# Kernel optimization log

Measured on AMD Instinct MI355X. Metric: run time of the kernel, lower is better.

Reference implementation:

```python
import jax, jax.numpy as jnp
import numpy as np

C = 256
CQ = C // 4


def setup_inputs() -> dict:
    key = jax.random.key(0)
    ks = jax.random.split(key, 7)
    B, H, W = 4, 64, 64
    x = jax.random.normal(ks[0], (B, C, H, W), dtype=jnp.float32)
    s = 1.0 / np.sqrt(C)
    Wq = jax.random.normal(ks[1], (CQ, C), dtype=jnp.float32) * s
    bq = jnp.zeros((CQ,), dtype=jnp.float32)
    Wk = jax.random.normal(ks[2], (CQ, C), dtype=jnp.float32) * s
    bk = jnp.zeros((CQ,), dtype=jnp.float32)
    Wv = jax.random.normal(ks[3], (C, C), dtype=jnp.float32) * s
    bv = jnp.zeros((C,), dtype=jnp.float32)
    gamma = jnp.zeros((1,), dtype=jnp.float32)
    return {"x": x, "Wq": Wq, "bq": bq, "Wk": Wk, "bk": bk,
            "Wv": Wv, "bv": bv, "gamma": gamma}


def reference(x, Wq, bq, Wk, bk, Wv, bv, gamma):
    B, Cc, Hh, Ww = x.shape
    N = Hh * Ww
    xf = x.reshape(B, Cc, N)                      # [B, C, N]
    # 1x1 convs are channel-mixing matmuls
    q = jnp.einsum('oc,bcn->bon', Wq, xf) + bq[None, :, None]   # [B, C/4, N]
    k = jnp.einsum('oc,bcn->bon', Wk, xf) + bk[None, :, None]   # [B, C/4, N]
    v = jnp.einsum('oc,bcn->bon', Wv, xf) + bv[None, :, None]   # [B, C, N]
    energy = jnp.einsum('bci,bcj->bij', q, k)     # [B, N, N] (unscaled)
    attn = jax.nn.softmax(energy, axis=-1)
    out = jnp.einsum('bcj,bij->bci', v, attn)     # [B, C, N]
    out = out.reshape(B, Cc, Hh, Ww)
    return gamma[0] * out + x
```

## Files before the change

### kernel.cpp

```cpp
#include <hip/hip_runtime.h>
#include <hip/hip_bf16.h>

typedef unsigned short u16;
typedef unsigned int u32;
typedef float f32x4 __attribute__((ext_vector_type(4)));
typedef short s16x8 __attribute__((ext_vector_type(8)));

#define MFMA16(a, b, c) __builtin_amdgcn_mfma_f32_16x16x32_bf16(a, b, c, 0, 0, 0)

#define NN 4096
#define CC 256
#define CQ 64

__device__ __forceinline__ u16 f2bf(float x) {
    union { float f; u32 u; } v; v.f = x;
    return (u16)((v.u + 0x7FFFu + ((v.u >> 16) & 1u)) >> 16);
}
__device__ __forceinline__ float bf2f(u16 u) {
    union { u32 u; float f; } v; v.u = ((u32)u) << 16;
    return v.f;
}
__device__ __forceinline__ void gll16(const void* g, void* l) {
    __builtin_amdgcn_global_load_lds(
        (const __attribute__((address_space(1))) void*)g,
        (__attribute__((address_space(3))) void*)l, 16, 0, 0);
}

__global__ __launch_bounds__(256) void prep(
    const float* __restrict__ x, const float* __restrict__ Wq,
    const float* __restrict__ Wk, const float* __restrict__ Wv,
    u16* __restrict__ xT, u16* __restrict__ wbf)
{
    const int bid = blockIdx.x, t = threadIdx.x;
    if (bid < 1024) {
        __shared__ float tile[64 * 65];
        const int b = bid >> 8, ctile = (bid >> 6) & 3, ntile = bid & 63;
        const int c0 = ctile * 64, n0 = ntile * 64;
        const int cw = t >> 4, nj = (t & 15) * 4;
        for (int it = 0; it < 4; it++) {
            const int ci = it * 16 + cw;
            const float4 v4 = *(const float4*)(x + ((size_t)(b * CC + c0 + ci)) * NN + n0 + nj);
            tile[(nj + 0) * 65 + ci] = v4.x;
            tile[(nj + 1) * 65 + ci] = v4.y;
            tile[(nj + 2) * 65 + ci] = v4.z;
            tile[(nj + 3) * 65 + ci] = v4.w;
        }
        __syncthreads();
        const int r = t >> 2, c16 = (t & 3) * 16;
        union { u16 h[16]; uint4 q[2]; } pk;
        for (int j = 0; j < 16; j++) pk.h[j] = f2bf(tile[r * 65 + c16 + j]);
        u16* dst = xT + ((size_t)(b * NN + n0 + r)) * CC + c0 + c16;
        *(uint4*)dst = pk.q[0];
        *(uint4*)(dst + 8) = pk.q[1];
    } else {
        const int flat = (bid - 1024) * 1024 + t * 4;
        const int o = flat >> 8, c = flat & 255;
        const float* src = (o < 64)  ? (Wq + (size_t)o * CC + c)
                         : (o < 128) ? (Wk + (size_t)(o - 64) * CC + c)
                                     : (Wv + (size_t)(o - 128) * CC + c);
        const float4 v4 = *(const float4*)src;
        union { u16 h[4]; uint2 d; } pk;
        pk.h[0] = f2bf(v4.x); pk.h[1] = f2bf(v4.y);
        pk.h[2] = f2bf(v4.z); pk.h[3] = f2bf(v4.w);
        *(uint2*)(wbf + (size_t)o * CC + c) = pk.d;
    }
}

__global__ __launch_bounds__(512, 4) void qkv(
    const u16* __restrict__ xT, const u16* __restrict__ wbf,
    const float* __restrict__ bq, const float* __restrict__ bk,
    const float* __restrict__ bv,
    u16* __restrict__ qT, u16* __restrict__ kT, u16* __restrict__ v)
{
    __shared__ __align__(16) u16 sm[384 * 64 + 32 * 64];
    u16* Ws = sm;
    u16* Xs = sm + 384 * 64;

    const int bid = blockIdx.x;
    const int b = bid >> 7, n0 = (bid & 127) * 32;
    const int t = threadIdx.x, lane = t & 63, w = t >> 6;
    const int col = lane & 15, quad = lane >> 4;

    f32x4 acc[3][2];
    for (int i = 0; i < 3; i++) { acc[i][0] = f32x4{0,0,0,0}; acc[i][1] = f32x4{0,0,0,0}; }

    for (int cc = 0; cc < 4; cc++) {
        const int c0 = cc * 64;
        for (int m = 0; m < 6; m++) {
            const int g = m * 512 + t;
            const int row = g >> 3, ch = g & 7;
            gll16(wbf + (size_t)row * CC + c0 + ((ch ^ (row & 7)) * 8), Ws + g * 8);
        }
        if (w < 4) {
            const int g = w * 64 + lane;
            const int n = g >> 3, ch = g & 7;
            gll16(xT + ((size_t)(b * NN + n0 + n)) * CC + c0 + ((ch ^ (n & 7)) * 8),
                  Xs + g * 8);
        }
        __syncthreads();
        for (int kk = 0; kk < 2; kk++) {
            s16x8 bx[2];
            for (int nt2 = 0; nt2 < 2; nt2++) {
                const int n = nt2 * 16 + col;
                bx[nt2] = *(const s16x8*)&Xs[n * 64 + (((kk * 4 + quad) ^ (n & 7)) * 8)];
            }
            for (int ot = 0; ot < 3; ot++) {
                const int row = w * 48 + ot * 16 + col;
                const s16x8 a = *(const s16x8*)&Ws[row * 64 + (((kk * 4 + quad) ^ (row & 7)) * 8)];
                acc[ot][0] = MFMA16(a, bx[0], acc[ot][0]);
                acc[ot][1] = MFMA16(a, bx[1], acc[ot][1]);
            }
        }
        __syncthreads();
    }
    for (int ot = 0; ot < 3; ot++) {
        const int og = w * 48 + ot * 16 + quad * 4;
        for (int nt2 = 0; nt2 < 2; nt2++) {
            const int n = n0 + nt2 * 16 + col;
            if (og < 64) {
                union { u16 h[4]; uint2 d; } pk;
                for (int r = 0; r < 4; r++) pk.h[r] = f2bf(acc[ot][nt2][r] + bq[og + r]);
                *(uint2*)(qT + ((size_t)(b * NN + n)) * CQ + og) = pk.d;
            } else if (og < 128) {
                union { u16 h[4]; uint2 d; } pk;
                for (int r = 0; r < 4; r++) pk.h[r] = f2bf(acc[ot][nt2][r] + bk[og - 64 + r]);
                *(uint2*)(kT + ((size_t)(b * NN + n)) * CQ + (og - 64)) = pk.d;
            } else {
                for (int r = 0; r < 4; r++)
                    v[((size_t)(b * CC + og - 128 + r)) * NN + n] =
                        f2bf(acc[ot][nt2][r] + bv[og - 128 + r]);
            }
        }
    }
}

__global__ __launch_bounds__(512, 4) void flash_attn(
    const u16* __restrict__ qT, const u16* __restrict__ kT,
    const u16* __restrict__ v,
    u16* __restrict__ Op0, float* __restrict__ Op1,
    float* __restrict__ lws)
{
    __shared__ __align__(16) u16 sm[25600];
    __shared__ float ls[2][64];

    const int bid = blockIdx.x;
    const int p = bid & 7;
    const int b = p >> 1, jh = p & 1;
    const int n0 = (bid >> 3) * 64;
    const int jb = jh * 2048;
    const int t = threadIdx.x;
    const int lane = t & 63, wv = t >> 6;
    const int col = lane & 15, quad = lane >> 4;
    const int strip = wv & 3, jhi = wv >> 2;
    const int ih = wv >> 2, cq = wv & 3;

    s16x8 aq[2];
    {
        const u16* qp = qT + ((size_t)(b * NN + n0 + strip * 16 + col)) * CQ + quad * 8;
        aq[0] = *(const s16x8*)qp;
        aq[1] = *(const s16x8*)(qp + 32);
    }

    f32x4 o_[2][4];
    for (int i = 0; i < 2; i++) for (int j = 0; j < 4; j++) o_[i][j] = f32x4{0,0,0,0};
    float lac[4] = {0.f, 0.f, 0.f, 0.f};

    const int kg = wv * 64 + lane;
    const int krow = kg >> 3;
    const u16* ksrc = kT + ((size_t)(b * NN + jb + krow)) * CQ + (((kg & 7) ^ (krow & 7)) * 8);
    const int kdo = kg * 8;
    const u16* vsrc[2];
    int vdo[2];
    for (int m = 0; m < 2; m++) {
        const int g = m * 512 + t;
        const int row = g >> 2;
        vdo[m] = g * 8;
        vsrc[m] = v + ((size_t)(b * CC + row)) * NN + jb + (g & 3) * 8;
    }

    auto issueK = [&](int jt, int kb) {
        if (wv < 4) gll16(ksrc + (size_t)jt * 32 * CQ, sm + kb * 2048 + kdo);
    };
    auto issueV = [&](int jt, int vb) {
        u16* base = sm + 4096 + vb * 8192;
        for (int m = 0; m < 2; m++)
            gll16(vsrc[m] + jt * 32, base + vdo[m]);
    };
    auto S_phase = [&](int kb, int pb) {
        const u16* Kb = sm + kb * 2048;
        u16* Pb = sm + 20480 + pb * 2560;
        f32x4 s = f32x4{0,0,0,0};
        for (int kk = 0; kk < 2; kk++) {
            const int jrow = jhi * 16 + col;
            const s16x8 bk_ = *(const s16x8*)
                &Kb[jrow * 64 + (((kk * 4 + quad) ^ (jrow & 7)) * 8)];
            s = MFMA16(aq[kk], bk_, s);
        }
        for (int r = 0; r < 4; r++) {
            const float pv = __expf(fminf(s[r], 60.f));
            lac[r] += pv;
            Pb[(strip * 16 + quad * 4 + r) * 40 + jhi * 16 + col] = f2bf(pv);
        }
    };
    auto PV_phase = [&](int pb, int vb) {
        const u16* Pb = sm + 20480 + pb * 2560;
        const u16* Vb = sm + 4096 + vb * 8192;
        s16x8 pa[2];
        for (int it2 = 0; it2 < 2; it2++)
            pa[it2] = *(const s16x8*)&Pb[((ih * 2 + it2) * 16 + col) * 40 + quad * 8];
        for (int ct = 0; ct < 4; ct++) {
            const int c = cq * 64 + ct * 16 + col;
            const s16x8 bv_ = *(const s16x8*)&Vb[c * 32 + quad * 8];
            o_[0][ct] = MFMA16(pa[0], bv_, o_[0][ct]);
            o_[1][ct] = MFMA16(pa[1], bv_, o_[1][ct]);
        }
    };

    issueK(0, 0);
    issueV(0, 0);
    issueK(1, 1);
    __syncthreads();
    S_phase(0, 0);

    int vcur = 0, pcur = 0;
    for (int m = 0; m < 64; m++) {
        __syncthreads();
        issueV((m + 1 < 64) ? m + 1 : 63, vcur ^ 1);
        issueK((m + 2 < 64) ? m + 2 : 63, m & 1);
        PV_phase(pcur, vcur);
        if (m < 63) S_phase((m + 1) & 1, pcur ^ 1);
        vcur ^= 1; pcur ^= 1;
    }

    for (int r = 0; r < 4; r++) {
        float lv = lac[r];
        lv += __shfl_xor(lv, 1, 64);
        lv += __shfl_xor(lv, 2, 64);
        lv += __shfl_xor(lv, 4, 64);
        lv += __shfl_xor(lv, 8, 64);
        lac[r] = lv;
    }
    if (col == 0)
        for (int r = 0; r < 4; r++)
            ls[jhi][strip * 16 + quad * 4 + r] = lac[r];
    __syncthreads();
    if (t < 64)
        lws[(size_t)jh * 4 * NN + (size_t)b * NN + n0 + t] = ls[0][t] + ls[1][t];

    float* Tf = (float*)sm;
    u16*  Tu = sm;
    for (int rd = 0; rd < 2; rd++) {
        if ((cq >> 1) == rd) {
            const int cl = (cq & 1) * 64;
            for (int it2 = 0; it2 < 2; it2++) {
                const int ib = (ih * 2 + it2) * 16 + quad * 4;
                for (int ct = 0; ct < 4; ct++) {
                    const int c = cl + ct * 16 + col;
                    if (jh == 0) {
                        union { u16 h[4]; uint2 d; } pk;
                        for (int r = 0; r < 4; r++) pk.h[r] = f2bf(o_[it2][ct][r]);
                        *(uint2*)&Tu[c * 136 + ib] = pk.d;
                    } else {
                        *(float2*)&Tf[c * 68 + ib] = float2{o_[it2][ct][0], o_[it2][ct][1]};
                        *(float2*)&Tf[c * 68 + ib + 2] = float2{o_[it2][ct][2], o_[it2][ct][3]};
                    }
                }
            }
        }
        __syncthreads();
        const int cl = t >> 2, i0 = (t & 3) * 16;
        const int c = rd * 128 + cl;
        if (jh == 0) {
            u16* dst = Op0 + ((size_t)(b * CC + c)) * NN + n0 + i0;
            *(uint4*)dst       = *(const uint4*)&Tu[cl * 136 + i0];
            *(uint4*)(dst + 8) = *(const uint4*)&Tu[cl * 136 + i0 + 8];
        } else {
            float* dst = Op1 + ((size_t)(b * CC + c)) * NN + n0 + i0;
            for (int k = 0; k < 4; k++)
                *(float4*)(dst + k * 4) = *(const float4*)&Tf[cl * 68 + i0 + k * 4];
        }
        __syncthreads();
    }
}

__global__ __launch_bounds__(256) void combine(
    const float* __restrict__ x, const u16* __restrict__ Op0,
    const float* __restrict__ lws, const float* __restrict__ gamma,
    float* __restrict__ out)
{
    const size_t idx = ((size_t)blockIdx.x * 256 + threadIdx.x) * 4;
    const int b = (int)(idx >> 20);
    const int n = (int)(idx & (NN - 1));
    const float g = gamma[0];
    const float4 xv = *(const float4*)(x + idx);
    const float4 o1 = *(const float4*)(out + idx);
    const u16* o0p = Op0 + idx;
    const float4 l0 = *(const float4*)(lws + (size_t)b * NN + n);
    const float4 l1 = *(const float4*)(lws + (size_t)4 * NN + (size_t)b * NN + n);
    float4 r;
    r.x = xv.x + g * (bf2f(o0p[0]) + o1.x) / (l0.x + l1.x);
    r.y = xv.y + g * (bf2f(o0p[1]) + o1.y) / (l0.y + l1.y);
    r.z = xv.z + g * (bf2f(o0p[2]) + o1.z) / (l0.z + l1.z);
    r.w = xv.w + g * (bf2f(o0p[3]) + o1.w) / (l0.w + l1.w);
    *(float4*)(out + idx) = r;
}

extern "C" void kernel_launch(void* const* d_in, const int* in_sizes, int n_in,
                              void* d_out, int out_size, void* d_ws, size_t ws_size,
                              hipStream_t stream)
{
    const float* x     = (const float*)d_in[0];
    const float* Wq    = (const float*)d_in[1];
    const float* bq    = (const float*)d_in[2];
    const float* Wk    = (const float*)d_in[3];
    const float* bk    = (const float*)d_in[4];
    const float* Wv    = (const float*)d_in[5];
    const float* bv    = (const float*)d_in[6];
    const float* gamma = (const float*)d_in[7];
    float* out = (float*)d_out;

    u16* xT  = (u16*)d_ws;
    u16* wbf = xT  + (size_t)4 * NN * CC;
    u16* qTw = wbf + (size_t)384 * CC;
    u16* kTw = qTw + (size_t)4 * NN * CQ;
    u16* vw  = kTw + (size_t)4 * NN * CQ;
    u16* Op0 = xT;
    float* lws = (float*)wbf;

    prep<<<1120, 256, 0, stream>>>(x, Wq, Wk, Wv, xT, wbf);
    qkv<<<512, 512, 0, stream>>>(xT, wbf, bq, bk, bv, qTw, kTw, vw);
    flash_attn<<<512, 512, 0, stream>>>(qTw, kTw, vw, Op0, out, lws);
    combine<<<4096, 256, 0, stream>>>(x, Op0, lws, gamma, out);
}
```

Before: 169.9 us.

## Fuse all four kernels into a persistent megakernel with grid barriers

Merges prep, qkv, flash attention and combine into one persistent kernel of 512 blocks, separated by atomic-counter grid barriers, so three launch gaps and kernel tails disappear. It also XOR-swizzles the V tile in LDS to cut bank conflicts, and switches P to truncating bf16 conversion to save ALU work. The barrier relies on all 512 blocks being co-resident; if they are not, the kernel deadlocks. The work is also redistributed differently in the prep and combine phases.

```diff
diff --git a/kernel.cpp b/kernel.cpp
--- a/kernel.cpp
+++ b/kernel.cpp
@@ -11,10 +11,15 @@
 #define NN 4096
 #define CC 256
 #define CQ 64
+#define NBLK 512
 
 __device__ __forceinline__ u16 f2bf(float x) {
     union { float f; u32 u; } v; v.f = x;
     return (u16)((v.u + 0x7FFFu + ((v.u >> 16) & 1u)) >> 16);
+}
+__device__ __forceinline__ u16 f2bf_t(float x) {
+    union { float f; u32 u; } v; v.f = x;
+    return (u16)(v.u >> 16);
 }
 __device__ __forceinline__ float bf2f(u16 u) {
     union { u32 u; float f; } v; v.u = ((u32)u) << 16;
@@ -26,19 +31,28 @@
         (__attribute__((address_space(3))) void*)l, 16, 0, 0);
 }
 
-__global__ __launch_bounds__(256) void prep(
-    const float* __restrict__ x, const float* __restrict__ Wq,
-    const float* __restrict__ Wk, const float* __restrict__ Wv,
-    u16* __restrict__ xT, u16* __restrict__ wbf)
-{
-    const int bid = blockIdx.x, t = threadIdx.x;
-    if (bid < 1024) {
-        __shared__ float tile[64 * 65];
-        const int b = bid >> 8, ctile = (bid >> 6) & 3, ntile = bid & 63;
+__device__ __forceinline__ void gbar(int* cnt) {
+    __syncthreads();
+    if (threadIdx.x == 0) {
+        __hip_atomic_fetch_add(cnt, 1, __ATOMIC_RELEASE, __HIP_MEMORY_SCOPE_AGENT);
+        while (__hip_atomic_load(cnt, __ATOMIC_ACQUIRE, __HIP_MEMORY_SCOPE_AGENT) < NBLK)
+            __builtin_amdgcn_s_sleep(2);
+    }
+    __syncthreads();
+}
+
+__device__ void phase_prep(const float* __restrict__ x, const float* __restrict__ Wq,
+                           const float* __restrict__ Wk, const float* __restrict__ Wv,
+                           u16* __restrict__ xT, u16* __restrict__ wbf, u16* SMEM)
+{
+    const int t = threadIdx.x;
+    float* tile = (float*)SMEM;
+    for (int u = blockIdx.x; u < 1024; u += NBLK) {
+        const int b = u >> 8, ctile = (u >> 6) & 3, ntile = u & 63;
         const int c0 = ctile * 64, n0 = ntile * 64;
-        const int cw = t >> 4, nj = (t & 15) * 4;
-        for (int it = 0; it < 4; it++) {
-            const int ci = it * 16 + cw;
+        for (int it = 0; it < 2; it++) {
+            const int idx = it * 512 + t;
+            const int ci = idx >> 4, nj = (idx & 15) * 4;
             const float4 v4 = *(const float4*)(x + ((size_t)(b * CC + c0 + ci)) * NN + n0 + nj);
             tile[(nj + 0) * 65 + ci] = v4.x;
             tile[(nj + 1) * 65 + ci] = v4.y;
@@ -46,14 +60,14 @@
             tile[(nj + 3) * 65 + ci] = v4.w;
         }
         __syncthreads();
-        const int r = t >> 2, c16 = (t & 3) * 16;
-        union { u16 h[16]; uint4 q[2]; } pk;
-        for (int j = 0; j < 16; j++) pk.h[j] = f2bf(tile[r * 65 + c16 + j]);
-        u16* dst = xT + ((size_t)(b * NN + n0 + r)) * CC + c0 + c16;
-        *(uint4*)dst = pk.q[0];
-        *(uint4*)(dst + 8) = pk.q[1];
-    } else {
-        const int flat = (bid - 1024) * 1024 + t * 4;
+        const int r = t >> 3, c8 = (t & 7) * 8;
+        union { u16 h[8]; uint4 q; } pk;
+        for (int j = 0; j < 8; j++) pk.h[j] = f2bf(tile[r * 65 + c8 + j]);
+        *(uint4*)(xT + ((size_t)(b * NN + n0 + r)) * CC + c0 + c8) = pk.q;
+        __syncthreads();
+    }
+    if (blockIdx.x < 48) {
+        const int flat = blockIdx.x * 2048 + t * 4;
         const int o = flat >> 8, c = flat & 255;
         const float* src = (o < 64)  ? (Wq + (size_t)o * CC + c)
                          : (o < 128) ? (Wk + (size_t)(o - 64) * CC + c)
@@ -66,15 +80,14 @@
     }
 }
 
-__global__ __launch_bounds__(512, 4) void qkv(
-    const u16* __restrict__ xT, const u16* __restrict__ wbf,
-    const float* __restrict__ bq, const float* __restrict__ bk,
-    const float* __restrict__ bv,
-    u16* __restrict__ qT, u16* __restrict__ kT, u16* __restrict__ v)
-{
-    __shared__ __align__(16) u16 sm[384 * 64 + 32 * 64];
-    u16* Ws = sm;
-    u16* Xs = sm + 384 * 64;
+__device__ void phase_qkv(const u16* __restrict__ xT, const u16* __restrict__ wbf,
+                          const float* __restrict__ bq, const float* __restrict__ bk,
+                          const float* __restrict__ bv,
+                          u16* __restrict__ qT, u16* __restrict__ kT,
+                          u16* __restrict__ v, u16* SMEM)
+{
+    u16* Ws = SMEM;
+    u16* Xs = SMEM + 384 * 64;
 
     const int bid = blockIdx.x;
     const int b = bid >> 7, n0 = (bid & 127) * 32;
@@ -134,14 +147,13 @@
     }
 }
 
-__global__ __launch_bounds__(512, 4) void flash_attn(
-    const u16* __restrict__ qT, const u16* __restrict__ kT,
-    const u16* __restrict__ v,
-    u16* __restrict__ Op0, float* __restrict__ Op1,
-    float* __restrict__ lws)
-{
-    __shared__ __align__(16) u16 sm[25600];
-    __shared__ float ls[2][64];
+__device__ void phase_flash(const u16* __restrict__ qT, const u16* __restrict__ kT,
+                            const u16* __restrict__ v,
+                            u16* __restrict__ Op0, float* __restrict__ Op1,
+                            float* __restrict__ lws, u16* SMEM)
+{
+    u16* sm = SMEM;
+    float* ls = (float*)(SMEM + 25600);
 
     const int bid = blockIdx.x;
     const int p = bid & 7;
@@ -153,6 +165,7 @@
     const int col = lane & 15, quad = lane >> 4;
     const int strip = wv & 3, jhi = wv >> 2;
     const int ih = wv >> 2, cq = wv & 3;
+    const int key2 = (col >> 1) & 3;
 
     s16x8 aq[2];
     {
@@ -174,8 +187,9 @@
     for (int m = 0; m < 2; m++) {
         const int g = m * 512 + t;
         const int row = g >> 2;
+        const int chc = (g & 3) ^ ((row >> 1) & 3);
         vdo[m] = g * 8;
-        vsrc[m] = v + ((size_t)(b * CC + row)) * NN + jb + (g & 3) * 8;
+        vsrc[m] = v + ((size_t)(b * CC + row)) * NN + jb + chc * 8;
     }
 
     auto issueK = [&](int jt, int kb) {
@@ -199,7 +213,7 @@
         for (int r = 0; r < 4; r++) {
             const float pv = __expf(fminf(s[r], 60.f));
             lac[r] += pv;
-            Pb[(strip * 16 + quad * 4 + r) * 40 + jhi * 16 + col] = f2bf(pv);
+            Pb[(strip * 16 + quad * 4 + r) * 40 + jhi * 16 + col] = f2bf_t(pv);
         }
     };
     auto PV_phase = [&](int pb, int vb) {
@@ -210,7 +224,7 @@
             pa[it2] = *(const s16x8*)&Pb[((ih * 2 + it2) * 16 + col) * 40 + quad * 8];
         for (int ct = 0; ct < 4; ct++) {
             const int c = cq * 64 + ct * 16 + col;
-            const s16x8 bv_ = *(const s16x8*)&Vb[c * 32 + quad * 8];
+            const s16x8 bv_ = *(const s16x8*)&Vb[c * 32 + ((quad ^ key2) * 8)];
             o_[0][ct] = MFMA16(pa[0], bv_, o_[0][ct]);
             o_[1][ct] = MFMA16(pa[1], bv_, o_[1][ct]);
         }
@@ -242,10 +256,10 @@
     }
     if (col == 0)
         for (int r = 0; r < 4; r++)
-            ls[jhi][strip * 16 + quad * 4 + r] = lac[r];
+            ls[jhi * 64 + strip * 16 + quad * 4 + r] = lac[r];
     __syncthreads();
     if (t < 64)
-        lws[(size_t)jh * 4 * NN + (size_t)b * NN + n0 + t] = ls[0][t] + ls[1][t];
+        lws[(size_t)jh * 4 * NN + (size_t)b * NN + n0 + t] = ls[t] + ls[64 + t];
 
     float* Tf = (float*)sm;
     u16*  Tu = sm;
@@ -283,26 +297,46 @@
     }
 }
 
-__global__ __launch_bounds__(256) void combine(
-    const float* __restrict__ x, const u16* __restrict__ Op0,
-    const float* __restrict__ lws, const float* __restrict__ gamma,
-    float* __restrict__ out)
-{
-    const size_t idx = ((size_t)blockIdx.x * 256 + threadIdx.x) * 4;
-    const int b = (int)(idx >> 20);
-    const int n = (int)(idx & (NN - 1));
+__device__ void phase_combine(const float* __restrict__ x, const u16* __restrict__ Op0,
+                              const float* __restrict__ lws, const float* __restrict__ gamma,
+                              float* __restrict__ out)
+{
     const float g = gamma[0];
-    const float4 xv = *(const float4*)(x + idx);
-    const float4 o1 = *(const float4*)(out + idx);
-    const u16* o0p = Op0 + idx;
-    const float4 l0 = *(const float4*)(lws + (size_t)b * NN + n);
-    const float4 l1 = *(const float4*)(lws + (size_t)4 * NN + (size_t)b * NN + n);
-    float4 r;
-    r.x = xv.x + g * (bf2f(o0p[0]) + o1.x) / (l0.x + l1.x);
-    r.y = xv.y + g * (bf2f(o0p[1]) + o1.y) / (l0.y + l1.y);
-    r.z = xv.z + g * (bf2f(o0p[2]) + o1.z) / (l0.z + l1.z);
-    r.w = xv.w + g * (bf2f(o0p[3]) + o1.w) / (l0.w + l1.w);
-    *(float4*)(out + idx) = r;
+    for (int pass = 0; pass < 4; pass++) {
+        const size_t idx = ((size_t)pass * 262144 + (size_t)blockIdx.x * 512 + threadIdx.x) * 4;
+        const int b = (int)(idx >> 20);
+        const int n = (int)(idx & (NN - 1));
+        const float4 xv = *(const float4*)(x + idx);
+        const float4 o1 = *(const float4*)(out + idx);
+        const uint2 o0 = *(const uint2*)(Op0 + idx);
+        const float4 l0 = *(const float4*)(lws + (size_t)b * NN + n);
+        const float4 l1 = *(const float4*)(lws + (size_t)4 * NN + (size_t)b * NN + n);
+        float4 r;
+        r.x = xv.x + g * (bf2f((u16)(o0.x & 0xffff))  + o1.x) / (l0.x + l1.x);
+        r.y = xv.y + g * (bf2f((u16)(o0.x >> 16))     + o1.y) / (l0.y + l1.y);
+        r.z = xv.z + g * (bf2f((u16)(o0.y & 0xffff))  + o1.z) / (l0.z + l1.z);
+        r.w = xv.w + g * (bf2f((u16)(o0.y >> 16))     + o1.w) / (l0.w + l1.w);
+        *(float4*)(out + idx) = r;
+    }
+}
+
+__global__ __launch_bounds__(512, 4) void pam_mega(
+    const float* __restrict__ x, const float* __restrict__ Wq,
+    const float* __restrict__ bq, const float* __restrict__ Wk,
+    const float* __restrict__ bk, const float* __restrict__ Wv,
+    const float* __restrict__ bv, const float* __restrict__ gamma,
+    u16* xT, u16* wbf, u16* qT, u16* kT, u16* v,
+    float* lws, int* ctr, float* out)
+{
+    __shared__ __align__(16) u16 SMEM[26624];
+
+    phase_prep(x, Wq, Wk, Wv, xT, wbf, SMEM);
+    gbar(ctr + 0);
+    phase_qkv(xT, wbf, bq, bk, bv, qT, kT, v, SMEM);
+    gbar(ctr + 1);
+    phase_flash(qT, kT, v, xT, out, lws, SMEM);
+    gbar(ctr + 2);
+    phase_combine(x, xT, lws, gamma, out);
 }
 
 extern "C" void kernel_launch(void* const* d_in, const int* in_sizes, int n_in,
@@ -321,14 +355,13 @@
 
     u16* xT  = (u16*)d_ws;
     u16* wbf = xT  + (size_t)4 * NN * CC;
-    u16* qTw = wbf + (size_t)384 * CC;
-    u16* kTw = qTw + (size_t)4 * NN * CQ;
-    u16* vw  = kTw + (size_t)4 * NN * CQ;
-    u16* Op0 = xT;
+    u16* qT  = wbf + (size_t)384 * CC;
+    u16* kT  = qT  + (size_t)4 * NN * CQ;
+    u16* vw  = kT  + (size_t)4 * NN * CQ;
+    int* ctr = (int*)(vw + (size_t)4 * CC * NN);
     float* lws = (float*)wbf;
 
-    prep<<<1120, 256, 0, stream>>>(x, Wq, Wk, Wv, xT, wbf);
-    qkv<<<512, 512, 0, stream>>>(xT, wbf, bq, bk, bv, qTw, kTw, vw);
-    flash_attn<<<512, 512, 0, stream>>>(qTw, kTw, vw, Op0, out, lws);
-    combine<<<4096, 256, 0, stream>>>(x, Op0, lws, gamma, out);
-}
+    hipMemsetAsync(ctr, 0, 3 * sizeof(int), stream);
+    pam_mega<<<NBLK, 512, 0, stream>>>(x, Wq, bq, Wk, bk, Wv, bv, gamma,
+                                       xT, wbf, qT, kT, vw, lws, ctr, out);
+}
```

Result: slower. 371.6 us (+118.7%).

## Fuse combine into flash_attn via inter-block flag handoff, swizzle V LDS

Applied to the files above, without the earlier changes.

Removes the separate combine kernel. The jh=1 block waits on a per-tile flag released by the jh=0 block, then merges both partial outputs, normalises by the summed row sums, applies gamma and adds x, writing the final output directly. This drops the fp32 partial round-trip through global memory and one kernel launch. It also XOR-swizzles the V tile in LDS to cut bank conflicts and switches P to truncating bf16 conversion. The spin-wait relies on the paired blocks being co-resident, which carries a deadlock risk, and it adds a memset launch.

```diff
diff --git a/kernel.cpp b/kernel.cpp
--- a/kernel.cpp
+++ b/kernel.cpp
@@ -15,6 +15,10 @@
 __device__ __forceinline__ u16 f2bf(float x) {
     union { float f; u32 u; } v; v.f = x;
     return (u16)((v.u + 0x7FFFu + ((v.u >> 16) & 1u)) >> 16);
+}
+__device__ __forceinline__ u16 f2bf_t(float x) {
+    union { float f; u32 u; } v; v.f = x;
+    return (u16)(v.u >> 16);
 }
 __device__ __forceinline__ float bf2f(u16 u) {
     union { u32 u; float f; } v; v.u = ((u32)u) << 16;
@@ -136,23 +140,27 @@
 
 __global__ __launch_bounds__(512, 4) void flash_attn(
     const u16* __restrict__ qT, const u16* __restrict__ kT,
-    const u16* __restrict__ v,
-    u16* __restrict__ Op0, float* __restrict__ Op1,
-    float* __restrict__ lws)
+    const u16* __restrict__ v, const float* __restrict__ x,
+    const float* __restrict__ gamma,
+    u16* __restrict__ Op0, float* __restrict__ lws,
+    int* __restrict__ flag, float* __restrict__ out)
 {
     __shared__ __align__(16) u16 sm[25600];
-    __shared__ float ls[2][64];
+    __shared__ float ls[128];
+    __shared__ float linv[64];
 
     const int bid = blockIdx.x;
     const int p = bid & 7;
     const int b = p >> 1, jh = p & 1;
-    const int n0 = (bid >> 3) * 64;
+    const int qt = bid >> 3;
+    const int n0 = qt * 64;
     const int jb = jh * 2048;
     const int t = threadIdx.x;
     const int lane = t & 63, wv = t >> 6;
     const int col = lane & 15, quad = lane >> 4;
     const int strip = wv & 3, jhi = wv >> 2;
     const int ih = wv >> 2, cq = wv & 3;
+    const int key2 = (col >> 1) & 3;
 
     s16x8 aq[2];
     {
@@ -174,8 +182,9 @@
     for (int m = 0; m < 2; m++) {
         const int g = m * 512 + t;
         const int row = g >> 2;
+        const int chc = (g & 3) ^ ((row >> 1) & 3);
         vdo[m] = g * 8;
-        vsrc[m] = v + ((size_t)(b * CC + row)) * NN + jb + (g & 3) * 8;
+        vsrc[m] = v + ((size_t)(b * CC + row)) * NN + jb + chc * 8;
     }
 
     auto issueK = [&](int jt, int kb) {
@@ -199,7 +208,7 @@
         for (int r = 0; r < 4; r++) {
             const float pv = __expf(fminf(s[r], 60.f));
             lac[r] += pv;
-            Pb[(strip * 16 + quad * 4 + r) * 40 + jhi * 16 + col] = f2bf(pv);
+            Pb[(strip * 16 + quad * 4 + r) * 40 + jhi * 16 + col] = f2bf_t(pv);
         }
     };
     auto PV_phase = [&](int pb, int vb) {
@@ -210,7 +219,7 @@
             pa[it2] = *(const s16x8*)&Pb[((ih * 2 + it2) * 16 + col) * 40 + quad * 8];
         for (int ct = 0; ct < 4; ct++) {
             const int c = cq * 64 + ct * 16 + col;
-            const s16x8 bv_ = *(const s16x8*)&Vb[c * 32 + quad * 8];
+            const s16x8 bv_ = *(const s16x8*)&Vb[c * 32 + ((quad ^ key2) * 8)];
             o_[0][ct] = MFMA16(pa[0], bv_, o_[0][ct]);
             o_[1][ct] = MFMA16(pa[1], bv_, o_[1][ct]);
         }
@@ -242,67 +251,82 @@
     }
     if (col == 0)
         for (int r = 0; r < 4; r++)
-            ls[jhi][strip * 16 + quad * 4 + r] = lac[r];
+            ls[jhi * 64 + strip * 16 + quad * 4 + r] = lac[r];
     __syncthreads();
-    if (t < 64)
-        lws[(size_t)jh * 4 * NN + (size_t)b * NN + n0 + t] = ls[0][t] + ls[1][t];
-
-    float* Tf = (float*)sm;
-    u16*  Tu = sm;
-    for (int rd = 0; rd < 2; rd++) {
-        if ((cq >> 1) == rd) {
-            const int cl = (cq & 1) * 64;
-            for (int it2 = 0; it2 < 2; it2++) {
-                const int ib = (ih * 2 + it2) * 16 + quad * 4;
-                for (int ct = 0; ct < 4; ct++) {
-                    const int c = cl + ct * 16 + col;
-                    if (jh == 0) {
+
+    const int fid = qt * 4 + b;
+    if (jh == 0) {
+        if (t < 64)
+            lws[(size_t)b * NN + n0 + t] = ls[t] + ls[64 + t];
+        u16* Tu = sm;
+        for (int rd = 0; rd < 2; rd++) {
+            if ((cq >> 1) == rd) {
+                const int cl = (cq & 1) * 64;
+                for (int it2 = 0; it2 < 2; it2++) {
+                    const int ib = (ih * 2 + it2) * 16 + quad * 4;
+                    for (int ct = 0; ct < 4; ct++) {
+                        const int c = cl + ct * 16 + col;
                         union { u16 h[4]; uint2 d; } pk;
                         for (int r = 0; r < 4; r++) pk.h[r] = f2bf(o_[it2][ct][r]);
                         *(uint2*)&Tu[c * 136 + ib] = pk.d;
-                    } else {
-                        *(float2*)&Tf[c * 68 + ib] = float2{o_[it2][ct][0], o_[it2][ct][1]};
+                    }
+                }
+            }
+            __syncthreads();
+            const int cl = t >> 2, i0 = (t & 3) * 16;
+            const int c = rd * 128 + cl;
+            u16* dst = Op0 + ((size_t)(b * CC + c)) * NN + n0 + i0;
+            *(uint4*)dst       = *(const uint4*)&Tu[cl * 136 + i0];
+            *(uint4*)(dst + 8) = *(const uint4*)&Tu[cl * 136 + i0 + 8];
+            __syncthreads();
+        }
+        if (t == 0)
+            __hip_atomic_store(&flag[fid], 1, __ATOMIC_RELEASE, __HIP_MEMORY_SCOPE_AGENT);
+    } else {
+        if (t == 0) {
+            while (__hip_atomic_load(&flag[fid], __ATOMIC_RELAXED,
+                                     __HIP_MEMORY_SCOPE_AGENT) == 0)
+                __builtin_amdgcn_s_sleep(1);
+            (void)__hip_atomic_load(&flag[fid], __ATOMIC_ACQUIRE,
+                                    __HIP_MEMORY_SCOPE_AGENT);
+        }
+        __syncthreads();
+        if (t < 64)
+            linv[t] = gamma[0] / (lws[(size_t)b * NN + n0 + t] + ls[t] + ls[64 + t]);
+        __syncthreads();
+        float* Tf = (float*)sm;
+        for (int rd = 0; rd < 2; rd++) {
+            if ((cq >> 1) == rd) {
+                const int cl = (cq & 1) * 64;
+                for (int it2 = 0; it2 < 2; it2++) {
+                    const int ib = (ih * 2 + it2) * 16 + quad * 4;
+                    for (int ct = 0; ct < 4; ct++) {
+                        const int c = cl + ct * 16 + col;
+                        *(float2*)&Tf[c * 68 + ib]     = float2{o_[it2][ct][0], o_[it2][ct][1]};
                         *(float2*)&Tf[c * 68 + ib + 2] = float2{o_[it2][ct][2], o_[it2][ct][3]};
                     }
                 }
             }
-        }
-        __syncthreads();
-        const int cl = t >> 2, i0 = (t & 3) * 16;
-        const int c = rd * 128 + cl;
-        if (jh == 0) {
-            u16* dst = Op0 + ((size_t)(b * CC + c)) * NN + n0 + i0;
-            *(uint4*)dst       = *(const uint4*)&Tu[cl * 136 + i0];
-            *(uint4*)(dst + 8) = *(const uint4*)&Tu[cl * 136 + i0 + 8];
-        } else {
-            float* dst = Op1 + ((size_t)(b * CC + c)) * NN + n0 + i0;
-            for (int k = 0; k < 4; k++)
-                *(float4*)(dst + k * 4) = *(const float4*)&Tf[cl * 68 + i0 + k * 4];
-        }
-        __syncthreads();
-    }
-}
-
-__global__ __launch_bounds__(256) void combine(
-    const float* __restrict__ x, const u16* __restrict__ Op0,
-    const float* __restrict__ lws, const float* __restrict__ gamma,
-    float* __restrict__ out)
-{
-    const size_t idx = ((size_t)blockIdx.x * 256 + threadIdx.x) * 4;
-    const int b = (int)(idx >> 20);
-    const int n = (int)(idx & (NN - 1));
-    const float g = gamma[0];
-    const float4 xv = *(const float4*)(x + idx);
-    const float4 o1 = *(const float4*)(out + idx);
-    const u16* o0p = Op0 + idx;
-    const float4 l0 = *(const float4*)(lws + (size_t)b * NN + n);
-    const float4 l1 = *(const float4*)(lws + (size_t)4 * NN + (size_t)b * NN + n);
-    float4 r;
-    r.x = xv.x + g * (bf2f(o0p[0]) + o1.x) / (l0.x + l1.x);
-    r.y = xv.y + g * (bf2f(o0p[1]) + o1.y) / (l0.y + l1.y);
-    r.z = xv.z + g * (bf2f(o0p[2]) + o1.z) / (l0.z + l1.z);
-    r.w = xv.w + g * (bf2f(o0p[3]) + o1.w) / (l0.w + l1.w);
-    *(float4*)(out + idx) = r;
+            __syncthreads();
+            const int cl = t >> 2, i0 = (t & 3) * 16;
+            const int c = rd * 128 + cl;
+            const u16* o0p = Op0 + ((size_t)(b * CC + c)) * NN + n0 + i0;
+            const float* xp = x + ((size_t)(b * CC + c)) * NN + n0 + i0;
+            float* op = out + ((size_t)(b * CC + c)) * NN + n0 + i0;
+            for (int k = 0; k < 4; k++) {
+                const float4 xv = *(const float4*)(xp + k * 4);
+                const float4 o1 = *(const float4*)&Tf[cl * 68 + i0 + k * 4];
+                const float4 li = *(const float4*)&linv[i0 + k * 4];
+                float4 r;
+                r.x = xv.x + (bf2f(o0p[k * 4 + 0]) + o1.x) * li.x;
+                r.y = xv.y + (bf2f(o0p[k * 4 + 1]) + o1.y) * li.y;
+                r.z = xv.z + (bf2f(o0p[k * 4 + 2]) + o1.z) * li.z;
+                r.w = xv.w + (bf2f(o0p[k * 4 + 3]) + o1.w) * li.w;
+                *(float4*)(op + k * 4) = r;
+            }
+            __syncthreads();
+        }
+    }
 }
 
 extern "C" void kernel_launch(void* const* d_in, const int* in_sizes, int n_in,
@@ -324,11 +348,12 @@
     u16* qTw = wbf + (size_t)384 * CC;
     u16* kTw = qTw + (size_t)4 * NN * CQ;
     u16* vw  = kTw + (size_t)4 * NN * CQ;
+    int* flags = (int*)(vw + (size_t)4 * CC * NN);
     u16* Op0 = xT;
     float* lws = (float*)wbf;
 
+    hipMemsetAsync(flags, 0, 256 * sizeof(int), stream);
     prep<<<1120, 256, 0, stream>>>(x, Wq, Wk, Wv, xT, wbf);
     qkv<<<512, 512, 0, stream>>>(xT, wbf, bq, bk, bv, qTw, kTw, vw);
-    flash_attn<<<512, 512, 0, stream>>>(qTw, kTw, vw, Op0, out, lws);
-    combine<<<4096, 256, 0, stream>>>(x, Op0, lws, gamma, out);
-}
+    flash_attn<<<512, 512, 0, stream>>>(qTw, kTw, vw, x, gamma, Op0, lws, flags, out);
+}
```

New measurement: 183.7 us. 8.1% more time.

## Fuse bf16 prep into QKV projection and swizzle V tile in attention

Applied to the files above, without the earlier changes.

Removes the separate prep kernel. The QKV projection now reads fp32 x and weights directly, transposes x through a padded LDS tile, and converts to bf16 in registers before the MFMAs. This drops one launch and the round trip of the bf16 transposed copy through global memory, at the cost of redundant weight loads and conversions in every block. In flash attention, the V tile load and read are XOR-swizzled to avoid LDS bank conflicts, and the P values are converted to bf16 by truncation instead of round-to-nearest, which cuts ALU work but adds a small rounding bias.

```diff
diff --git a/kernel.cpp b/kernel.cpp
--- a/kernel.cpp
+++ b/kernel.cpp
@@ -16,6 +16,10 @@
     union { float f; u32 u; } v; v.f = x;
     return (u16)((v.u + 0x7FFFu + ((v.u >> 16) & 1u)) >> 16);
 }
+__device__ __forceinline__ u16 f2bf_t(float x) {
+    union { float f; u32 u; } v; v.f = x;
+    return (u16)(v.u >> 16);
+}
 __device__ __forceinline__ float bf2f(u16 u) {
     union { u32 u; float f; } v; v.u = ((u32)u) << 16;
     return v.f;
@@ -25,56 +29,24 @@
         (const __attribute__((address_space(1))) void*)g,
         (__attribute__((address_space(3))) void*)l, 16, 0, 0);
 }
-
-__global__ __launch_bounds__(256) void prep(
+__device__ __forceinline__ s16x8 pk8(float a0, float a1, float a2, float a3,
+                                     float a4, float a5, float a6, float a7) {
+    union { __hip_bfloat162 h[4]; s16x8 v8; } u;
+    u.h[0] = __float22bfloat162_rn(float2{a0, a1});
+    u.h[1] = __float22bfloat162_rn(float2{a2, a3});
+    u.h[2] = __float22bfloat162_rn(float2{a4, a5});
+    u.h[3] = __float22bfloat162_rn(float2{a6, a7});
+    return u.v8;
+}
+
+__global__ __launch_bounds__(512, 4) void qkv(
     const float* __restrict__ x, const float* __restrict__ Wq,
     const float* __restrict__ Wk, const float* __restrict__ Wv,
-    u16* __restrict__ xT, u16* __restrict__ wbf)
-{
-    const int bid = blockIdx.x, t = threadIdx.x;
-    if (bid < 1024) {
-        __shared__ float tile[64 * 65];
-        const int b = bid >> 8, ctile = (bid >> 6) & 3, ntile = bid & 63;
-        const int c0 = ctile * 64, n0 = ntile * 64;
-        const int cw = t >> 4, nj = (t & 15) * 4;
-        for (int it = 0; it < 4; it++) {
-            const int ci = it * 16 + cw;
-            const float4 v4 = *(const float4*)(x + ((size_t)(b * CC + c0 + ci)) * NN + n0 + nj);
-            tile[(nj + 0) * 65 + ci] = v4.x;
-            tile[(nj + 1) * 65 + ci] = v4.y;
-            tile[(nj + 2) * 65 + ci] = v4.z;
-            tile[(nj + 3) * 65 + ci] = v4.w;
-        }
-        __syncthreads();
-        const int r = t >> 2, c16 = (t & 3) * 16;
-        union { u16 h[16]; uint4 q[2]; } pk;
-        for (int j = 0; j < 16; j++) pk.h[j] = f2bf(tile[r * 65 + c16 + j]);
-        u16* dst = xT + ((size_t)(b * NN + n0 + r)) * CC + c0 + c16;
-        *(uint4*)dst = pk.q[0];
-        *(uint4*)(dst + 8) = pk.q[1];
-    } else {
-        const int flat = (bid - 1024) * 1024 + t * 4;
-        const int o = flat >> 8, c = flat & 255;
-        const float* src = (o < 64)  ? (Wq + (size_t)o * CC + c)
-                         : (o < 128) ? (Wk + (size_t)(o - 64) * CC + c)
-                                     : (Wv + (size_t)(o - 128) * CC + c);
-        const float4 v4 = *(const float4*)src;
-        union { u16 h[4]; uint2 d; } pk;
-        pk.h[0] = f2bf(v4.x); pk.h[1] = f2bf(v4.y);
-        pk.h[2] = f2bf(v4.z); pk.h[3] = f2bf(v4.w);
-        *(uint2*)(wbf + (size_t)o * CC + c) = pk.d;
-    }
-}
-
-__global__ __launch_bounds__(512, 4) void qkv(
-    const u16* __restrict__ xT, const u16* __restrict__ wbf,
     const float* __restrict__ bq, const float* __restrict__ bk,
     const float* __restrict__ bv,
     u16* __restrict__ qT, u16* __restrict__ kT, u16* __restrict__ v)
 {
-    __shared__ __align__(16) u16 sm[384 * 64 + 32 * 64];
-    u16* Ws = sm;
-    u16* Xs = sm + 384 * 64;
+    __shared__ __align__(16) float Xf[64 * 34];
 
     const int bid = blockIdx.x;
     const int b = bid >> 7, n0 = (bid & 127) * 32;
@@ -84,34 +56,48 @@
     f32x4 acc[3][2];
     for (int i = 0; i < 3; i++) { acc[i][0] = f32x4{0,0,0,0}; acc[i][1] = f32x4{0,0,0,0}; }
 
+    const int xc = t >> 3, xs = (t & 7) * 4;
+    const float* xbase = x + ((size_t)(b * CC + xc)) * NN + n0 + xs;
+    float4 xr = *(const float4*)xbase;
+
+    const float* wb_[3];
+    for (int ot = 0; ot < 3; ot++) {
+        const int og = w * 48 + ot * 16;
+        wb_[ot] = (og < 64)  ? Wq + (size_t)(og + col) * CC
+                : (og < 128) ? Wk + (size_t)(og - 64 + col) * CC
+                             : Wv + (size_t)(og - 128 + col) * CC;
+    }
+
     for (int cc = 0; cc < 4; cc++) {
         const int c0 = cc * 64;
-        for (int m = 0; m < 6; m++) {
-            const int g = m * 512 + t;
-            const int row = g >> 3, ch = g & 7;
-            gll16(wbf + (size_t)row * CC + c0 + ((ch ^ (row & 7)) * 8), Ws + g * 8);
-        }
-        if (w < 4) {
-            const int g = w * 64 + lane;
-            const int n = g >> 3, ch = g & 7;
-            gll16(xT + ((size_t)(b * NN + n0 + n)) * CC + c0 + ((ch ^ (n & 7)) * 8),
-                  Xs + g * 8);
-        }
+        __syncthreads();
+        *(float2*)&Xf[xc * 34 + xs]     = float2{xr.x, xr.y};
+        *(float2*)&Xf[xc * 34 + xs + 2] = float2{xr.z, xr.w};
+        if (cc < 3)
+            xr = *(const float4*)(xbase + (size_t)(cc + 1) * 64 * NN);
+        float4 wr[3][2][2];
+        for (int ot = 0; ot < 3; ot++)
+            for (int kk = 0; kk < 2; kk++) {
+                const float* wp = wb_[ot] + c0 + kk * 32 + quad * 8;
+                wr[ot][kk][0] = *(const float4*)wp;
+                wr[ot][kk][1] = *(const float4*)(wp + 4);
+            }
         __syncthreads();
         for (int kk = 0; kk < 2; kk++) {
             s16x8 bx[2];
             for (int nt2 = 0; nt2 < 2; nt2++) {
-                const int n = nt2 * 16 + col;
-                bx[nt2] = *(const s16x8*)&Xs[n * 64 + (((kk * 4 + quad) ^ (n & 7)) * 8)];
+                const float* xp = &Xf[(kk * 32 + quad * 8) * 34 + nt2 * 16 + col];
+                bx[nt2] = pk8(xp[0], xp[34], xp[68], xp[102],
+                              xp[136], xp[170], xp[204], xp[238]);
             }
             for (int ot = 0; ot < 3; ot++) {
-                const int row = w * 48 + ot * 16 + col;
-                const s16x8 a = *(const s16x8*)&Ws[row * 64 + (((kk * 4 + quad) ^ (row & 7)) * 8)];
+                const float* f0 = (const float*)&wr[ot][kk][0];
+                const s16x8 a = pk8(f0[0], f0[1], f0[2], f0[3],
+                                    f0[4], f0[5], f0[6], f0[7]);
                 acc[ot][0] = MFMA16(a, bx[0], acc[ot][0]);
                 acc[ot][1] = MFMA16(a, bx[1], acc[ot][1]);
             }
         }
-        __syncthreads();
     }
     for (int ot = 0; ot < 3; ot++) {
         const int og = w * 48 + ot * 16 + quad * 4;
@@ -141,7 +127,7 @@
     float* __restrict__ lws)
 {
     __shared__ __align__(16) u16 sm[25600];
-    __shared__ float ls[2][64];
+    __shared__ float ls[128];
 
     const int bid = blockIdx.x;
     const int p = bid & 7;
@@ -153,6 +139,7 @@
     const int col = lane & 15, quad = lane >> 4;
     const int strip = wv & 3, jhi = wv >> 2;
     const int ih = wv >> 2, cq = wv & 3;
+    const int key2 = (col >> 1) & 3;
 
     s16x8 aq[2];
     {
@@ -174,8 +161,9 @@
     for (int m = 0; m < 2; m++) {
         const int g = m * 512 + t;
         const int row = g >> 2;
+        const int chc = (g & 3) ^ ((row >> 1) & 3);
         vdo[m] = g * 8;
-        vsrc[m] = v + ((size_t)(b * CC + row)) * NN + jb + (g & 3) * 8;
+        vsrc[m] = v + ((size_t)(b * CC + row)) * NN + jb + chc * 8;
     }
 
     auto issueK = [&](int jt, int kb) {
@@ -199,7 +187,7 @@
         for (int r = 0; r < 4; r++) {
             const float pv = __expf(fminf(s[r], 60.f));
             lac[r] += pv;
-            Pb[(strip * 16 + quad * 4 + r) * 40 + jhi * 16 + col] = f2bf(pv);
+            Pb[(strip * 16 + quad * 4 + r) * 40 + jhi * 16 + col] = f2bf_t(pv);
         }
     };
     auto PV_phase = [&](int pb, int vb) {
@@ -210,7 +198,7 @@
             pa[it2] = *(const s16x8*)&Pb[((ih * 2 + it2) * 16 + col) * 40 + quad * 8];
         for (int ct = 0; ct < 4; ct++) {
             const int c = cq * 64 + ct * 16 + col;
-            const s16x8 bv_ = *(const s16x8*)&Vb[c * 32 + quad * 8];
+            const s16x8 bv_ = *(const s16x8*)&Vb[c * 32 + ((quad ^ key2) * 8)];
             o_[0][ct] = MFMA16(pa[0], bv_, o_[0][ct]);
             o_[1][ct] = MFMA16(pa[1], bv_, o_[1][ct]);
         }
@@ -242,10 +230,10 @@
     }
     if (col == 0)
         for (int r = 0; r < 4; r++)
-            ls[jhi][strip * 16 + quad * 4 + r] = lac[r];
+            ls[jhi * 64 + strip * 16 + quad * 4 + r] = lac[r];
     __syncthreads();
     if (t < 64)
-        lws[(size_t)jh * 4 * NN + (size_t)b * NN + n0 + t] = ls[0][t] + ls[1][t];
+        lws[(size_t)jh * 4 * NN + (size_t)b * NN + n0 + t] = ls[t] + ls[64 + t];
 
     float* Tf = (float*)sm;
     u16*  Tu = sm;
@@ -261,7 +249,7 @@
                         for (int r = 0; r < 4; r++) pk.h[r] = f2bf(o_[it2][ct][r]);
                         *(uint2*)&Tu[c * 136 + ib] = pk.d;
                     } else {
-                        *(float2*)&Tf[c * 68 + ib] = float2{o_[it2][ct][0], o_[it2][ct][1]};
+                        *(float2*)&Tf[c * 68 + ib]     = float2{o_[it2][ct][0], o_[it2][ct][1]};
                         *(float2*)&Tf[c * 68 + ib + 2] = float2{o_[it2][ct][2], o_[it2][ct][3]};
                     }
                 }
@@ -319,16 +307,13 @@
     const float* gamma = (const float*)d_in[7];
     float* out = (float*)d_out;
 
-    u16* xT  = (u16*)d_ws;
-    u16* wbf = xT  + (size_t)4 * NN * CC;
-    u16* qTw = wbf + (size_t)384 * CC;
+    u16* Op0 = (u16*)d_ws;
+    float* lws = (float*)(Op0 + (size_t)4 * NN * CC);
+    u16* qTw = (u16*)(lws + (size_t)8 * NN);
     u16* kTw = qTw + (size_t)4 * NN * CQ;
     u16* vw  = kTw + (size_t)4 * NN * CQ;
-    u16* Op0 = xT;
-    float* lws = (float*)wbf;
-
-    prep<<<1120, 256, 0, stream>>>(x, Wq, Wk, Wv, xT, wbf);
-    qkv<<<512, 512, 0, stream>>>(xT, wbf, bq, bk, bv, qTw, kTw, vw);
+
+    qkv<<<512, 512, 0, stream>>>(x, Wq, Wk, Wv, bq, bk, bv, qTw, kTw, vw);
     flash_attn<<<512, 512, 0, stream>>>(qTw, kTw, vw, Op0, out, lws);
     combine<<<4096, 256, 0, stream>>>(x, Op0, lws, gamma, out);
 }
```

Measured after the change: 179.3 us. +5.5%, slower.
